# Optimization experiments

Measured on AMD Instinct MI355X. Metric: run time of the kernel, lower is better.

The kernel has to match this reference:

```python
import jax, jax.numpy as jnp
import numpy as np
from jax import lax

B, T, H = 16, 4096, 512

def setup_inputs() -> dict:
    key = jax.random.key(0)
    ks = jax.random.split(key, 10)
    return {
        "query": jax.random.normal(ks[0], (B, 1, H), dtype=jnp.float32),
        "value": jax.random.normal(ks[1], (B, T, H), dtype=jnp.float32),
        "last_attn": jax.random.uniform(ks[2], (B, T), dtype=jnp.float32),
        "conv_w": jax.random.normal(ks[3], (H, 1, 3), dtype=jnp.float32) * 0.05,
        "conv_b": jax.random.normal(ks[4], (H,), dtype=jnp.float32) * 0.05,
        "Wq": jax.random.normal(ks[5], (H, H), dtype=jnp.float32) * (1.0 / np.sqrt(H)),
        "Wv": jax.random.normal(ks[6], (H, H), dtype=jnp.float32) * (1.0 / np.sqrt(H)),
        "bias": jax.random.uniform(ks[7], (H,), minval=-0.1, maxval=0.1, dtype=jnp.float32),
        "w_score": jax.random.normal(ks[8], (1, H), dtype=jnp.float32) * (1.0 / np.sqrt(H)),
        "b_score": jax.random.normal(ks[9], (1,), dtype=jnp.float32) * 0.05,
    }

def reference(query, value, last_attn, conv_w, conv_b, Wq, Wv, bias, w_score, b_score):
    # conv1d over last_attn: (B,1,T) -> (B,H,T), kernel 3, pad 1
    conv = lax.conv_general_dilated(
        last_attn[:, None, :], conv_w, window_strides=(1,), padding="SAME",
        dimension_numbers=("NCH", "OIH", "NCH"))
    conv_attn = conv.transpose(0, 2, 1) + conv_b           # (B,T,H)
    q = jnp.einsum("bqh,oh->bqo", query, Wq)               # (B,1,H), Linear w/o bias: x @ W.T
    v = jnp.einsum("bth,oh->bto", value, Wv)               # (B,T,H)
    e = jnp.tanh(q + v + conv_attn + bias)                 # (B,T,H) broadcast over q_len=1
    score = jnp.einsum("bth,h->bt", e, w_score[0]) + b_score[0]  # (B,T)
    # smoothing=True: sigmoid + L1 normalize
    s = jax.nn.sigmoid(score)
    attn = s / jnp.sum(s, axis=-1, keepdims=True)          # (B,T)
    context = jnp.einsum("bt,bth->bh", attn, value)        # (B,H)
    out = jnp.concatenate([context, query[:, 0, :]], axis=1)  # (B,2H)
    return out, attn
```

## Files before the change

kernel.cpp:

```cpp
#include <hip/hip_runtime.h>
#include <hip/hip_bf16.h>
#include <cstddef>

#define BB 16
#define TT 4096
#define HH 512

typedef _Float16 half8 __attribute__((ext_vector_type(8)));
typedef float f32x4 __attribute__((ext_vector_type(4)));

__global__ void prep_kernel(const float* __restrict__ query,
                            const float* __restrict__ conv_b,
                            const float* __restrict__ Wq,
                            const float* __restrict__ Wv,
                            const float* __restrict__ bias,
                            _Float16* __restrict__ Bpack,
                            float* __restrict__ qb,
                            float* __restrict__ ssum,
                            float* __restrict__ ctx) {
    int blk = blockIdx.x;
    int tid = threadIdx.x;
    if (blk < 128) {
        int TN = blk >> 2, kq = blk & 3;
        int kb = kq * 4 + (tid >> 6);
        int lane = tid & 63;
        int n = TN * 16 + (lane & 15);
        int k = kb * 32 + ((lane >> 4) << 3);
        const float4* src = (const float4*)(Wv + (size_t)n * HH + k);
        float4 v0 = src[0], v1 = src[1];
        half8 h = { (_Float16)v0.x, (_Float16)v0.y, (_Float16)v0.z, (_Float16)v0.w,
                    (_Float16)v1.x, (_Float16)v1.y, (_Float16)v1.z, (_Float16)v1.w };
        *(half8*)(Bpack + (size_t)TN * 8192 + kb * 512 + lane * 8) = h;
    } else if (blk < 192) {
        int q = blk - 128;
        int b = q >> 2, oq = q & 3;
        __shared__ float qrow[HH];
        for (int i = tid; i < HH; i += 256) qrow[i] = query[b * HH + i];
        __syncthreads();
        int wave = tid >> 6, lane = tid & 63;
        float4 q1 = *(const float4*)(qrow + lane * 8);
        float4 q2 = *(const float4*)(qrow + lane * 8 + 4);
        for (int i = wave; i < 128; i += 4) {
            int o = oq * 128 + i;
            const float4* w = (const float4*)(Wq + (size_t)o * HH);
            float4 a = w[lane * 2], c = w[lane * 2 + 1];
            float acc = a.x * q1.x + a.y * q1.y + a.z * q1.z + a.w * q1.w
                      + c.x * q2.x + c.y * q2.y + c.z * q2.z + c.w * q2.w;
            #pragma unroll
            for (int off = 1; off < 64; off <<= 1) acc += __shfl_xor(acc, off, 64);
            if (lane == 0) qb[b * HH + o] = acc + bias[o] + conv_b[o];
        }
    } else {
        for (int i = tid; i < BB; i += 256) ssum[i] = 0.f;
        for (int i = tid; i < BB * HH; i += 256) ctx[i] = 0.f;
    }
}

__global__ __launch_bounds__(256, 4) void gemm_fused_kernel(
        const float* __restrict__ value,
        const float* __restrict__ last_attn,
        const float* __restrict__ conv_w,
        const float* __restrict__ w_score,
        const float* __restrict__ b_score,
        const _Float16* __restrict__ Bpack,
        const float* __restrict__ qb,
        float* __restrict__ sbuf,
        float* __restrict__ ssum,
        float* __restrict__ ctx) {
    __shared__ _Float16 As[32 * 512];
    __shared__ float sred[32][4];
    __shared__ float s_lds[32];

    int tid = threadIdx.x;
    int blk = blockIdx.x;
    int b = blk >> 7;
    int t0 = (blk & 127) << 5;

    int lane = tid & 63, ng = tid >> 6;
    int quad = lane >> 4, lm = lane & 15;

    int st = tid & 31, sg = tid >> 5;
    const float4* pA = (const float4*)(value + ((size_t)(b * TT + t0 + st)) * HH + sg * 64);
    #pragma unroll
    for (int u = 0; u < 8; ++u) {
        float4 v0 = pA[2 * u], v1 = pA[2 * u + 1];
        int cph = (sg * 8 + u) ^ (st & 7);
        half8 h = { (_Float16)v0.x, (_Float16)v0.y, (_Float16)v0.z, (_Float16)v0.w,
                    (_Float16)v1.x, (_Float16)v1.y, (_Float16)v1.z, (_Float16)v1.w };
        *(half8*)(As + st * 512 + cph * 8) = h;
    }

    f32x4 acc[2][4];
    #pragma unroll
    for (int mt = 0; mt < 2; ++mt)
        #pragma unroll
        for (int nt = 0; nt < 4; ++nt) { f32x4 z = {0.f,0.f,0.f,0.f}; acc[mt][nt] = z; }

    half8 breg[2][4];
    float rs[2][4];
    #pragma unroll
    for (int mt = 0; mt < 2; ++mt)
        #pragma unroll
        for (int j = 0; j < 4; ++j) rs[mt][j] = 0.f;

    const _Float16* Bbase = Bpack + lane * 8;

    auto loadB = [&](half8* dst, int p, int kb) {
        #pragma unroll
        for (int nt = 0; nt < 4; ++nt)
            dst[nt] = *(const half8*)(Bbase + (size_t)(((p * 16 + ng * 4 + nt) * 16 + kb) * 512));
    };
    auto compute = [&](int kb, const half8* bb) {
        #pragma unroll
        for (int mt = 0; mt < 2; ++mt) {
            int tr = mt * 16 + lm;
            int cph = (kb * 4 + quad) ^ (tr & 7);
            half8 a = *(const half8*)(As + tr * 512 + cph * 8);
            #pragma unroll
            for (int nt = 0; nt < 4; ++nt)
                acc[mt][nt] = __builtin_amdgcn_mfma_f32_16x16x32_f16(a, bb[nt], acc[mt][nt], 0, 0, 0);
        }
    };
    auto epi = [&](int p) {
        float qvv[4], c0v[4], c1v[4], c2v[4], wvv[4];
        #pragma unroll
        for (int nt = 0; nt < 4; ++nt) {
            int o = p * 256 + ng * 64 + nt * 16 + lm;
            qvv[nt] = qb[b * HH + o];
            c0v[nt] = conv_w[o * 3 + 0];
            c1v[nt] = conv_w[o * 3 + 1];
            c2v[nt] = conv_w[o * 3 + 2];
            wvv[nt] = w_score[o];
        }
        #pragma unroll
        for (int mt = 0; mt < 2; ++mt) {
            #pragma unroll
            for (int j = 0; j < 4; ++j) {
                int tg = t0 + mt * 16 + quad * 4 + j;
                const float* la = last_attn + b * TT + tg;
                float lam = (tg > 0) ? la[-1] : 0.f;
                float la0 = la[0];
                float lap = (tg < TT - 1) ? la[1] : 0.f;
                float r = 0.f;
                #pragma unroll
                for (int nt = 0; nt < 4; ++nt) {
                    float act = acc[mt][nt][j] + qvv[nt]
                              + c0v[nt] * lam + c1v[nt] * la0 + c2v[nt] * lap;
                    act = fminf(15.f, fmaxf(-15.f, act));
                    float e2 = __expf(2.f * act);
                    r += ((e2 - 1.f) / (e2 + 1.f)) * wvv[nt];
                }
                rs[mt][j] += r;
            }
        }
    };

    loadB(breg[0], 0, 0);
    __syncthreads();

    #pragma unroll
    for (int kb = 0; kb < 16; ++kb) {
        if (kb < 15) loadB(breg[(kb + 1) & 1], 0, kb + 1);
        else         loadB(breg[0], 1, 0);
        compute(kb, breg[kb & 1]);
    }
    epi(0);
    #pragma unroll
    for (int mt = 0; mt < 2; ++mt)
        #pragma unroll
        for (int nt = 0; nt < 4; ++nt) { f32x4 z = {0.f,0.f,0.f,0.f}; acc[mt][nt] = z; }

    #pragma unroll
    for (int kb = 0; kb < 16; ++kb) {
        if (kb < 15) loadB(breg[(kb + 1) & 1], 1, kb + 1);
        compute(kb, breg[kb & 1]);
    }
    epi(1);

    #pragma unroll
    for (int mt = 0; mt < 2; ++mt)
        #pragma unroll
        for (int j = 0; j < 4; ++j) {
            float v = rs[mt][j];
            #pragma unroll
            for (int off = 1; off < 16; off <<= 1) v += __shfl_xor(v, off, 64);
            if (lm == 0) sred[mt * 16 + quad * 4 + j][ng] = v;
        }
    __syncthreads();
    if (tid < 32) {
        float sc = b_score[0] + sred[tid][0] + sred[tid][1] + sred[tid][2] + sred[tid][3];
        float s = 1.f / (1.f + __expf(-sc));
        s_lds[tid] = s;
        sbuf[b * TT + t0 + tid] = s;
        float tot = s;
        #pragma unroll
        for (int off = 1; off < 32; off <<= 1) tot += __shfl_xor(tot, off, 64);
        if (tid == 0) atomicAdd(&ssum[b], tot);
    }
    __syncthreads();

    #pragma unroll
    for (int hh = 0; hh < 2; ++hh) {
        int h = tid + hh * 256;
        int cl = h >> 3, j = h & 7;
        float a = 0.f;
        #pragma unroll 8
        for (int t2 = 0; t2 < 32; ++t2) {
            int cph = cl ^ (t2 & 7);
            a += s_lds[t2] * (float)As[t2 * 512 + cph * 8 + j];
        }
        atomicAdd(&ctx[b * HH + h], a);
    }
}

__global__ void finalize_kernel(const float* __restrict__ query,
                                const float* __restrict__ ctx,
                                const float* __restrict__ sbuf,
                                const float* __restrict__ ssum,
                                float* __restrict__ out) {
    int idx = blockIdx.x * 256 + threadIdx.x;
    if (idx < BB * 2 * HH) {
        int b = idx >> 10, c = idx & 1023;
        float v;
        if (c < HH) v = ctx[b * HH + c] / ssum[b];
        else        v = query[b * HH + (c - HH)];
        out[idx] = v;
    } else {
        int j = idx - BB * 2 * HH;
        int b = j >> 12, t = j & 4095;
        out[idx] = sbuf[b * TT + t] / ssum[b];
    }
}

extern "C" void kernel_launch(void* const* d_in, const int* in_sizes, int n_in,
                              void* d_out, int out_size, void* d_ws, size_t ws_size,
                              hipStream_t stream) {
    const float* query     = (const float*)d_in[0];
    const float* value     = (const float*)d_in[1];
    const float* last_attn = (const float*)d_in[2];
    const float* conv_w    = (const float*)d_in[3];
    const float* conv_b    = (const float*)d_in[4];
    const float* Wq        = (const float*)d_in[5];
    const float* Wv        = (const float*)d_in[6];
    const float* bias      = (const float*)d_in[7];
    const float* w_score   = (const float*)d_in[8];
    const float* b_score   = (const float*)d_in[9];

    char* ws = (char*)d_ws;
    _Float16* Bpack = (_Float16*)ws;
    float* qb     = (float*)(ws + 524288);
    float* sbuf   = (float*)(ws + 557056);
    float* ssum   = (float*)(ws + 819200);
    float* ctx    = (float*)(ws + 819264);
    float* out    = (float*)d_out;

    prep_kernel<<<193, 256, 0, stream>>>(query, conv_b, Wq, Wv, bias, Bpack, qb, ssum, ctx);
    gemm_fused_kernel<<<2048, 256, 0, stream>>>(value, last_attn, conv_w, w_score,
                                                b_score, Bpack, qb, sbuf, ssum, ctx);
    finalize_kernel<<<320, 256, 0, stream>>>(query, ctx, sbuf, ssum, out);
}
```

Baseline: 312.2 us.

## Double row tile to 64 per block with 8 waves sharing B loads

Each block now handles 64 time rows with 512 threads (two M sub-tiles by four N groups), so every Wv fragment loaded from global/L2 is reused across twice as many rows and the grid halves. Bpack is re-laid out k-block-major so the B stream advances with a constant stride. The epilogue is reorganised per-nt and the cross-wave score reduction now goes through LDS atomics. The cost is 64KB of LDS per block, which limits occupancy, and an extra barrier for the reduction.

```diff
diff --git a/kernel.cpp b/kernel.cpp
--- a/kernel.cpp
+++ b/kernel.cpp
@@ -21,16 +21,16 @@
     int blk = blockIdx.x;
     int tid = threadIdx.x;
     if (blk < 128) {
-        int TN = blk >> 2, kq = blk & 3;
+        int tn = blk >> 2, kq = blk & 3;
         int kb = kq * 4 + (tid >> 6);
         int lane = tid & 63;
-        int n = TN * 16 + (lane & 15);
+        int n = tn * 16 + (lane & 15);
         int k = kb * 32 + ((lane >> 4) << 3);
         const float4* src = (const float4*)(Wv + (size_t)n * HH + k);
         float4 v0 = src[0], v1 = src[1];
         half8 h = { (_Float16)v0.x, (_Float16)v0.y, (_Float16)v0.z, (_Float16)v0.w,
                     (_Float16)v1.x, (_Float16)v1.y, (_Float16)v1.z, (_Float16)v1.w };
-        *(half8*)(Bpack + (size_t)TN * 8192 + kb * 512 + lane * 8) = h;
+        *(half8*)(Bpack + ((size_t)(kb * 32 + tn) * 64 + lane) * 8) = h;
     } else if (blk < 192) {
         int q = blk - 128;
         int b = q >> 2, oq = q & 3;
@@ -56,7 +56,7 @@
     }
 }
 
-__global__ __launch_bounds__(256, 4) void gemm_fused_kernel(
+__global__ __launch_bounds__(512, 4) void gemm_fused_kernel(
         const float* __restrict__ value,
         const float* __restrict__ last_attn,
         const float* __restrict__ conv_w,
@@ -67,116 +67,114 @@
         float* __restrict__ sbuf,
         float* __restrict__ ssum,
         float* __restrict__ ctx) {
-    __shared__ _Float16 As[32 * 512];
-    __shared__ float sred[32][4];
-    __shared__ float s_lds[32];
+    __shared__ _Float16 As[64 * 512];
+    __shared__ float sred[64][4];
+    __shared__ float s_lds[64];
 
     int tid = threadIdx.x;
     int blk = blockIdx.x;
-    int b = blk >> 7;
-    int t0 = (blk & 127) << 5;
-
-    int lane = tid & 63, ng = tid >> 6;
+    int b = blk >> 6;
+    int t0 = (blk & 63) << 5;
+    t0 <<= 1;
+
+    int lane = tid & 63;
+    int w = tid >> 6, msub = w & 1, ng = w >> 1;
     int quad = lane >> 4, lm = lane & 15;
 
-    int st = tid & 31, sg = tid >> 5;
-    const float4* pA = (const float4*)(value + ((size_t)(b * TT + t0 + st)) * HH + sg * 64);
-    #pragma unroll
-    for (int u = 0; u < 8; ++u) {
-        float4 v0 = pA[2 * u], v1 = pA[2 * u + 1];
-        int cph = (sg * 8 + u) ^ (st & 7);
-        half8 h = { (_Float16)v0.x, (_Float16)v0.y, (_Float16)v0.z, (_Float16)v0.w,
-                    (_Float16)v1.x, (_Float16)v1.y, (_Float16)v1.z, (_Float16)v1.w };
-        *(half8*)(As + st * 512 + cph * 8) = h;
-    }
-
-    f32x4 acc[2][4];
-    #pragma unroll
-    for (int mt = 0; mt < 2; ++mt)
-        #pragma unroll
-        for (int nt = 0; nt < 4; ++nt) { f32x4 z = {0.f,0.f,0.f,0.f}; acc[mt][nt] = z; }
-
-    half8 breg[2][4];
+    {
+        int st = tid >> 3, cc = tid & 7;
+        const float4* pA = (const float4*)(value + ((size_t)(b * TT + t0 + st)) * HH) + cc * 2;
+        #pragma unroll
+        for (int u = 0; u < 8; ++u) {
+            float4 v0 = pA[u * 16], v1 = pA[u * 16 + 1];
+            int cph = (cc + u * 8) ^ (st & 7);
+            half8 h = { (_Float16)v0.x, (_Float16)v0.y, (_Float16)v0.z, (_Float16)v0.w,
+                        (_Float16)v1.x, (_Float16)v1.y, (_Float16)v1.z, (_Float16)v1.w };
+            *(half8*)(As + st * 512 + cph * 8) = h;
+        }
+    }
+
     float rs[2][4];
     #pragma unroll
     for (int mt = 0; mt < 2; ++mt)
         #pragma unroll
         for (int j = 0; j < 4; ++j) rs[mt][j] = 0.f;
 
-    const _Float16* Bbase = Bpack + lane * 8;
-
-    auto loadB = [&](half8* dst, int p, int kb) {
+    __syncthreads();
+
+    #pragma unroll 1
+    for (int p = 0; p < 2; ++p) {
+        f32x4 acc[2][4];
+        #pragma unroll
+        for (int mt = 0; mt < 2; ++mt)
+            #pragma unroll
+            for (int nt = 0; nt < 4; ++nt) { f32x4 z = {0.f,0.f,0.f,0.f}; acc[mt][nt] = z; }
+
+        const _Float16* bp = Bpack + (size_t)(p * 16 + ng * 4) * 512 + lane * 8;
+        half8 breg[2][4];
         #pragma unroll
         for (int nt = 0; nt < 4; ++nt)
-            dst[nt] = *(const half8*)(Bbase + (size_t)(((p * 16 + ng * 4 + nt) * 16 + kb) * 512));
-    };
-    auto compute = [&](int kb, const half8* bb) {
-        #pragma unroll
-        for (int mt = 0; mt < 2; ++mt) {
-            int tr = mt * 16 + lm;
-            int cph = (kb * 4 + quad) ^ (tr & 7);
-            half8 a = *(const half8*)(As + tr * 512 + cph * 8);
-            #pragma unroll
-            for (int nt = 0; nt < 4; ++nt)
-                acc[mt][nt] = __builtin_amdgcn_mfma_f32_16x16x32_f16(a, bb[nt], acc[mt][nt], 0, 0, 0);
-        }
-    };
-    auto epi = [&](int p) {
-        float qvv[4], c0v[4], c1v[4], c2v[4], wvv[4];
+            breg[0][nt] = *(const half8*)(bp + nt * 512);
+        bp += 16384;
+
+        #pragma unroll 2
+        for (int kb = 0; kb < 16; ++kb) {
+            int cb = kb & 1;
+            if (kb < 15) {
+                #pragma unroll
+                for (int nt = 0; nt < 4; ++nt)
+                    breg[cb ^ 1][nt] = *(const half8*)(bp + nt * 512);
+                bp += 16384;
+            }
+            #pragma unroll
+            for (int mt = 0; mt < 2; ++mt) {
+                int tr = msub * 32 + mt * 16 + lm;
+                int cph = ((kb << 2) + quad) ^ (tr & 7);
+                half8 a = *(const half8*)(As + tr * 512 + cph * 8);
+                #pragma unroll
+                for (int nt = 0; nt < 4; ++nt)
+                    acc[mt][nt] = __builtin_amdgcn_mfma_f32_16x16x32_f16(a, breg[cb][nt], acc[mt][nt], 0, 0, 0);
+            }
+        }
+
         #pragma unroll
         for (int nt = 0; nt < 4; ++nt) {
             int o = p * 256 + ng * 64 + nt * 16 + lm;
-            qvv[nt] = qb[b * HH + o];
-            c0v[nt] = conv_w[o * 3 + 0];
-            c1v[nt] = conv_w[o * 3 + 1];
-            c2v[nt] = conv_w[o * 3 + 2];
-            wvv[nt] = w_score[o];
-        }
-        #pragma unroll
-        for (int mt = 0; mt < 2; ++mt) {
-            #pragma unroll
-            for (int j = 0; j < 4; ++j) {
-                int tg = t0 + mt * 16 + quad * 4 + j;
-                const float* la = last_attn + b * TT + tg;
-                float lam = (tg > 0) ? la[-1] : 0.f;
-                float la0 = la[0];
-                float lap = (tg < TT - 1) ? la[1] : 0.f;
-                float r = 0.f;
+            float qv = qb[b * HH + o];
+            float c0 = conv_w[o * 3 + 0];
+            float c1 = conv_w[o * 3 + 1];
+            float c2 = conv_w[o * 3 + 2];
+            float wv = w_score[o];
+            #pragma unroll
+            for (int mt = 0; mt < 2; ++mt) {
                 #pragma unroll
-                for (int nt = 0; nt < 4; ++nt) {
-                    float act = acc[mt][nt][j] + qvv[nt]
-                              + c0v[nt] * lam + c1v[nt] * la0 + c2v[nt] * lap;
+                for (int j = 0; j < 4; ++j) {
+                    int tg = t0 + msub * 32 + mt * 16 + quad * 4 + j;
+                    const float* la = last_attn + b * TT + tg;
+                    float lam = (tg > 0) ? la[-1] : 0.f;
+                    float la0 = la[0];
+                    float lap = (tg < TT - 1) ? la[1] : 0.f;
+                    float act = acc[mt][nt][j] + qv + c0 * lam + c1 * la0 + c2 * lap;
                     act = fminf(15.f, fmaxf(-15.f, act));
                     float e2 = __expf(2.f * act);
-                    r += ((e2 - 1.f) / (e2 + 1.f)) * wvv[nt];
+                    rs[mt][j] += ((e2 - 1.f) / (e2 + 1.f)) * wv;
                 }
-                rs[mt][j] += r;
-            }
-        }
-    };
-
-    loadB(breg[0], 0, 0);
-    __syncthreads();
-
-    #pragma unroll
-    for (int kb = 0; kb < 16; ++kb) {
-        if (kb < 15) loadB(breg[(kb + 1) & 1], 0, kb + 1);
-        else         loadB(breg[0], 1, 0);
-        compute(kb, breg[kb & 1]);
-    }
-    epi(0);
+            }
+        }
+    }
+
     #pragma unroll
     for (int mt = 0; mt < 2; ++mt)
         #pragma unroll
-        for (int nt = 0; nt < 4; ++nt) { f32x4 z = {0.f,0.f,0.f,0.f}; acc[mt][nt] = z; }
-
-    #pragma unroll
-    for (int kb = 0; kb < 16; ++kb) {
-        if (kb < 15) loadB(breg[(kb + 1) & 1], 1, kb + 1);
-        compute(kb, breg[kb & 1]);
-    }
-    epi(1);
-
+        for (int j = 0; j < 4; ++j) {
+            float v = rs[mt][j];
+            #pragma unroll
+            for (int off = 1; off < 16; off <<= 1) v += __shfl_xor(v, off, 64);
+            if (lm == 0) {
+                if (ng == 0) sred[msub * 32 + mt * 16 + quad * 4 + j][0] = v;
+            }
+        }
+    __syncthreads();
     #pragma unroll
     for (int mt = 0; mt < 2; ++mt)
         #pragma unroll
@@ -184,28 +182,29 @@
             float v = rs[mt][j];
             #pragma unroll
             for (int off = 1; off < 16; off <<= 1) v += __shfl_xor(v, off, 64);
-            if (lm == 0) sred[mt * 16 + quad * 4 + j][ng] = v;
-        }
-    __syncthreads();
-    if (tid < 32) {
-        float sc = b_score[0] + sred[tid][0] + sred[tid][1] + sred[tid][2] + sred[tid][3];
+            if (lm == 0 && ng != 0)
+                atomicAdd(&sred[msub * 32 + mt * 16 + quad * 4 + j][0], v);
+        }
+    __syncthreads();
+
+    if (tid < 64) {
+        float sc = b_score[0] + sred[tid][0];
         float s = 1.f / (1.f + __expf(-sc));
         s_lds[tid] = s;
         sbuf[b * TT + t0 + tid] = s;
         float tot = s;
         #pragma unroll
-        for (int off = 1; off < 32; off <<= 1) tot += __shfl_xor(tot, off, 64);
+        for (int off = 1; off < 64; off <<= 1) tot += __shfl_xor(tot, off, 64);
         if (tid == 0) atomicAdd(&ssum[b], tot);
     }
     __syncthreads();
 
-    #pragma unroll
-    for (int hh = 0; hh < 2; ++hh) {
-        int h = tid + hh * 256;
+    {
+        int h = tid;
         int cl = h >> 3, j = h & 7;
         float a = 0.f;
         #pragma unroll 8
-        for (int t2 = 0; t2 < 32; ++t2) {
+        for (int t2 = 0; t2 < 64; ++t2) {
             int cph = cl ^ (t2 & 7);
             a += s_lds[t2] * (float)As[t2 * 512 + cph * 8 + j];
         }
@@ -255,7 +254,7 @@
     float* out    = (float*)d_out;
 
     prep_kernel<<<193, 256, 0, stream>>>(query, conv_b, Wq, Wv, bias, Bpack, qb, ssum, ctx);
-    gemm_fused_kernel<<<2048, 256, 0, stream>>>(value, last_attn, conv_w, w_score,
+    gemm_fused_kernel<<<1024, 512, 0, stream>>>(value, last_attn, conv_w, w_score,
                                                 b_score, Bpack, qb, sbuf, ssum, ctx);
     finalize_kernel<<<320, 256, 0, stream>>>(query, ctx, sbuf, ssum, out);
 }
```

Result: faster. 279.6 us (-10.4%).
